# Performance work log

Measured on AMD Instinct MI355X. Metric: run time of the kernel, lower is better.

Reference implementation:

```python
import jax, jax.numpy as jnp
import numpy as np


def _euclidean_cdist(x, q):
    # torch.cdist with p=2: pairwise L2 distances, shape [B, Q]
    x2 = jnp.sum(x * x, axis=-1, keepdims=True)          # [B, 1]
    q2 = jnp.sum(q * q, axis=-1)[None, :]                # [1, Q]
    d2 = x2 + q2 - 2.0 * (x @ q.T)                        # [B, Q]
    return jnp.sqrt(jnp.maximum(d2, 0.0))


def setup_inputs() -> dict:
    key = jax.random.key(0)
    k1, k2 = jax.random.split(key)
    x = jax.random.normal(k1, (1024, 256), dtype=jnp.float32)
    queue = jax.random.normal(k2, (32768, 256), dtype=jnp.float32)
    return {"x": x, "queue": queue}


def reference(x, queue):
    # Queue update: concat then keep the newest max_size rows (queue assumed full)
    max_size = queue.shape[0]
    q = jnp.concatenate([queue, x], axis=0)[-max_size:]   # [Q, F]
    # Distance matrix + top-2 nearest (topk of negated distances)
    d = _euclidean_cdist(x, q)                            # [B, Q]
    _, idx = jax.lax.top_k(-d, 2)                         # [B, 2]
    # Second-nearest neighbor (first is the point itself, dist 0)
    return q[idx[:, 1]]                                   # [B, F]
```

## Files before the change

kernel.cpp:

```cpp
#include <hip/hip_runtime.h>
#include <stdint.h>

#define B_ROWS 1024
#define FEAT   256
#define QSZ    32768
#define SHIFT  1024
#define QX     (QSZ - B_ROWS)
#define BM     64
#define NGY    (QSZ / BM)
#define MARGIN 8.0f

typedef float  v4f __attribute__((ext_vector_type(4)));
typedef short  v8s __attribute__((ext_vector_type(8)));

__device__ __forceinline__ uint32_t key_flip(uint32_t u) {
    return u ^ ((uint32_t)((int32_t)u >> 31) | 0x80000000u);
}
__device__ __forceinline__ float key_m(uint32_t k) {
    uint32_t u = k & 0xFFFF8000u;
    u = (u & 0x80000000u) ? (u ^ 0x80000000u) : ~u;
    return __uint_as_float(u);
}
__device__ __forceinline__ void k2_insert(uint32_t& k1, uint32_t& k2, uint32_t key) {
    uint32_t hi = max(k1, key); k1 = min(k1, key); k2 = min(k2, hi);
}
__device__ __forceinline__ uint2 k2_merge(uint2 a, uint2 b) {
    uint32_t hi = max(a.x, b.x);
    uint2 r; r.x = min(a.x, b.x); r.y = min(min(a.y, b.y), hi);
    return r;
}

struct Top2 { float m1; int j1; float m2; int j2; };
__device__ __forceinline__ bool better(float ma, int ja, float mb, int jb) {
    return (ma < mb) || (ma == mb && ja < jb);
}
__device__ __forceinline__ void t2_insert(Top2& t, float m, int j) {
    if (better(m, j, t.m1, t.j1)) { t.m2 = t.m1; t.j2 = t.j1; t.m1 = m; t.j1 = j; }
    else if (better(m, j, t.m2, t.j2)) { t.m2 = m; t.j2 = j; }
}

__device__ __forceinline__ const float* q_row_ptr(int j, const float* x, const float* queue) {
    return (j < QX) ? (queue + (size_t)(j + SHIFT) * FEAT) : (x + (size_t)(j - QX) * FEAT);
}

__device__ __forceinline__ unsigned short f2bf(float f) {
    uint32_t u = __float_as_uint(f);
    uint32_t r = u + 0x7FFFu + ((u >> 16) & 1u);
    return (unsigned short)(r >> 16);
}

__device__ __forceinline__ void lds_load16(const void* g, void* l) {
    __builtin_amdgcn_global_load_lds(
        (const __attribute__((address_space(1))) uint32_t*)g,
        (__attribute__((address_space(3))) uint32_t*)l, 16, 0, 0);
}

__global__ __launch_bounds__(256) void convert_x(const float* __restrict__ x,
                                                 unsigned short* __restrict__ x_bf) {
    int wave = threadIdx.x >> 6, lane = threadIdx.x & 63;
    int r = blockIdx.x * 4 + wave;
    float4 v = ((const float4*)(x + (size_t)r * FEAT))[lane];
    ushort4 h;
    h.x = f2bf(v.x); h.y = f2bf(v.y); h.z = f2bf(v.z); h.w = f2bf(v.w);
    ((ushort4*)x_bf)[(size_t)r * 64 + lane] = h;
}

__global__ __launch_bounds__(256, 3) void nn_fused(const float* __restrict__ x,
                                                   const float* __restrict__ queue,
                                                   const unsigned short* __restrict__ x_bf,
                                                   float* __restrict__ q2,
                                                   uint2* __restrict__ partials) {
    __shared__ __align__(16) unsigned short As[BM * FEAT];
    __shared__ __align__(16) unsigned short Bs[2][128 * 32];
    __shared__ __align__(16) float sq2[BM];

    const int t    = threadIdx.x;
    const int w    = t >> 6, lane = t & 63;
    const int quad = lane >> 4, l16 = lane & 15;
    const int gy   = blockIdx.x;

    const int srow = lane >> 2;
    const int sgl  = (lane & 3) ^ ((lane >> 3) & 3);
    const unsigned short* gB0 = x_bf + (size_t)(w * 32 + srow) * FEAT + sgl * 8;
    lds_load16(gB0,             &Bs[0][(w * 32) * 32]);
    lds_load16(gB0 + 16 * FEAT, &Bs[0][(w * 32 + 16) * 32]);

    const int arow = t >> 2, aqtr = t & 3;
    const float* asrc = q_row_ptr(gy * BM + arow, x, queue) + aqtr * 64;
    float ss = 0.0f;
#pragma unroll
    for (int gi = 0; gi < 8; ++gi) {
        float4 a = *(const float4*)(asrc + gi * 8);
        float4 b = *(const float4*)(asrc + gi * 8 + 4);
        ss += a.x * a.x + a.y * a.y + a.z * a.z + a.w * a.w
            + b.x * b.x + b.y * b.y + b.z * b.z + b.w * b.w;
        uint32_t p0 = (uint32_t)f2bf(a.x) | ((uint32_t)f2bf(a.y) << 16);
        uint32_t p1 = (uint32_t)f2bf(a.z) | ((uint32_t)f2bf(a.w) << 16);
        uint32_t p2 = (uint32_t)f2bf(b.x) | ((uint32_t)f2bf(b.y) << 16);
        uint32_t p3 = (uint32_t)f2bf(b.z) | ((uint32_t)f2bf(b.w) << 16);
        const int g    = aqtr * 8 + gi;
        const int phys = (g & 24) | ((g & 7) ^ (arow & 7));
        *(uint4*)&As[arow * FEAT + phys * 8] = make_uint4(p0, p1, p2, p3);
    }
    ss += __shfl_xor(ss, 1, 64);
    ss += __shfl_xor(ss, 2, 64);
    if (aqtr == 0) { sq2[arow] = ss; q2[gy * BM + arow] = ss; }

    v4f acc[4][2];
#pragma unroll
    for (int a = 0; a < 4; ++a)
#pragma unroll
        for (int b = 0; b < 2; ++b) acc[a][b] = (v4f)0.0f;

    const int  gphysB = quad ^ ((l16 >> 1) & 3);
    const char* Brd = (const char*)&Bs[0][0] + (size_t)(w * 32 + l16) * 64 + gphysB * 16;

    __syncthreads();

    for (int gx = 0; gx < 8; ++gx) {
#pragma unroll
        for (int c = 0; c < 8; ++c) {
            const int m = gx * 8 + c;
            if (m < 63) {
                const int mm = m + 1;
                const unsigned short* gBn = gB0 + (size_t)(mm >> 3) * (128 * FEAT) + (mm & 7) * 32;
                unsigned short* dstb = &Bs[(c + 1) & 1][(w * 32) * 32];
                lds_load16(gBn,             dstb);
                lds_load16(gBn + 16 * FEAT, dstb + 16 * 32);
                __builtin_amdgcn_sched_barrier(0);
                asm volatile("s_waitcnt vmcnt(2)" ::: "memory");
            } else {
                __builtin_amdgcn_sched_barrier(0);
                asm volatile("s_waitcnt vmcnt(0)" ::: "memory");
            }
            __builtin_amdgcn_s_barrier();

            const int physA = ((c >> 1) * 8) | ((((c & 1) * 4) + quad) ^ (l16 & 7));
            v8s fa[4], fb[2];
#pragma unroll
            for (int tm = 0; tm < 4; ++tm)
                fa[tm] = *(const v8s*)((const char*)As + (size_t)(tm * 16 + l16) * 512 + physA * 16);
            const char* Bc = Brd + (c & 1) * 8192;
#pragma unroll
            for (int tn = 0; tn < 2; ++tn)
                fb[tn] = *(const v8s*)(Bc + tn * 1024);
            __builtin_amdgcn_s_setprio(1);
#pragma unroll
            for (int tm = 0; tm < 4; ++tm)
#pragma unroll
                for (int tn = 0; tn < 2; ++tn)
                    acc[tm][tn] = __builtin_amdgcn_mfma_f32_16x16x32_bf16(fa[tm], fb[tn], acc[tm][tn], 0, 0, 0);
            __builtin_amdgcn_s_setprio(0);
            __builtin_amdgcn_s_barrier();
        }

        float q2r[4][4];
#pragma unroll
        for (int tm = 0; tm < 4; ++tm) {
            v4f qq = *(const v4f*)&sq2[tm * 16 + quad * 4];
#pragma unroll
            for (int r = 0; r < 4; ++r) q2r[tm][r] = qq[r];
        }
        const int jbase = gy * BM + quad * 4;
#pragma unroll
        for (int tn = 0; tn < 2; ++tn) {
            uint32_t k1 = 0xFFFFFFFFu, k2 = 0xFFFFFFFFu;
#pragma unroll
            for (int tm = 0; tm < 4; ++tm)
#pragma unroll
                for (int r = 0; r < 4; ++r) {
                    float mv = fmaf(-2.0f, acc[tm][tn][r], q2r[tm][r]);
                    uint32_t u = key_flip(__float_as_uint(mv));
                    uint32_t key = (u & 0xFFFF8000u) | (uint32_t)(jbase + tm * 16 + r);
                    k2_insert(k1, k2, key);
                    acc[tm][tn][r] = 0.0f;
                }
#pragma unroll
            for (int mask = 16; mask <= 32; mask <<= 1) {
                uint32_t o1 = __shfl_xor(k1, mask, 64);
                uint32_t o2 = __shfl_xor(k2, mask, 64);
                uint32_t hi = max(k1, o1);
                k1 = min(k1, o1);
                k2 = min(min(k2, o2), hi);
            }
            if (quad == 0)
                partials[(size_t)(gx * 128 + w * 32 + tn * 16 + l16) * NGY + gy] = make_uint2(k1, k2);
        }
    }
}

__global__ __launch_bounds__(256) void nn_finalize(const float* __restrict__ x,
                                                   const float* __restrict__ queue,
                                                   const float* __restrict__ q2,
                                                   const uint2* __restrict__ partials,
                                                   float* __restrict__ out) {
    __shared__ float    xs[256];
    __shared__ uint2    red[256];
    __shared__ int      list[64];
    __shared__ float    escore[64];
    __shared__ int      s_cnt;
    __shared__ uint32_t s_kcut;
    __shared__ int      s_j2;

    const int t = threadIdx.x, i = blockIdx.x;
    const int w = t >> 6, lane = t & 63;

    xs[t] = x[(size_t)i * FEAT + t];
    uint2 pa = partials[(size_t)i * NGY + t];
    uint2 pb = partials[(size_t)i * NGY + 256 + t];
    uint2 pm = k2_merge(pa, pb);
    red[t] = pm;
    if (t == 0) s_cnt = 0;
    __syncthreads();

    if (w == 0) {
        uint2 a = red[lane];
        a = k2_merge(a, red[lane + 64]);
        a = k2_merge(a, red[lane + 128]);
        a = k2_merge(a, red[lane + 192]);
#pragma unroll
        for (int mask = 1; mask <= 32; mask <<= 1) {
            uint2 o;
            o.x = __shfl_xor(a.x, mask, 64);
            o.y = __shfl_xor(a.y, mask, 64);
            a = k2_merge(a, o);
        }
        if (lane == 0) {
            float cutf = key_m(a.y) + MARGIN;
            s_kcut = key_flip(__float_as_uint(cutf)) | 0x7FFFu;
        }
    }
    __syncthreads();
    uint32_t kcut = s_kcut;
    if (pm.x <= kcut) { int q_ = atomicAdd(&s_cnt, 1); if (q_ < 64) list[q_] = (int)(pm.x & 0x7FFFu); }
    if (pm.y <= kcut) { int q_ = atomicAdd(&s_cnt, 1); if (q_ < 64) list[q_] = (int)(pm.y & 0x7FFFu); }
    __syncthreads();
    int n = min(s_cnt, 64);

    for (int c = w; c < n; c += 4) {
        int j = list[c];
        const float4* qr = (const float4*)q_row_ptr(j, x, queue);
        float4 qv = qr[lane];
        float4 xv = ((const float4*)xs)[lane];
        float s = qv.x * xv.x + qv.y * xv.y + qv.z * xv.z + qv.w * xv.w;
#pragma unroll
        for (int off = 32; off; off >>= 1) s += __shfl_xor(s, off, 64);
        if (lane == 0) escore[c] = q2[j] - 2.0f * s;
    }
    __syncthreads();
    if (t == 0) {
        Top2 a;
        a.m1 = __builtin_inff(); a.j1 = 0x7FFFFFFF;
        a.m2 = __builtin_inff(); a.j2 = 0x7FFFFFFF;
        for (int c = 0; c < n; ++c) t2_insert(a, escore[c], list[c]);
        s_j2 = a.j2;
    }
    __syncthreads();
    out[(size_t)i * FEAT + t] = q_row_ptr(s_j2, x, queue)[t];
}

extern "C" void kernel_launch(void* const* d_in, const int* in_sizes, int n_in,
                              void* d_out, int out_size, void* d_ws, size_t ws_size,
                              hipStream_t stream) {
    const float* x     = (const float*)d_in[0];
    const float* queue = (const float*)d_in[1];

    unsigned short* x_bf     = (unsigned short*)d_ws;
    float*          q2       = (float*)((char*)d_ws + (1u << 20));
    uint2*          partials = (uint2*)((char*)d_ws + (2u << 20));

    convert_x<<<B_ROWS / 4, 256, 0, stream>>>(x, x_bf);
    nn_fused<<<NGY, 256, 0, stream>>>(x, queue, x_bf, q2, partials);
    nn_finalize<<<B_ROWS, 256, 0, stream>>>(x, queue, q2, partials, (float*)d_out);
}
```

Measured before the change: 119.0 us.

## Keep queue tile in registers and stream x_bf fragments directly from global

The GEMM kernel stops staging x_bf tiles through double-buffered LDS with global_load_lds and barriers. Instead each wave holds the full 64x256 queue tile fragments in registers and loads B fragments straight from global memory into registers, double-buffered across 16-column tiles, with each wave owning 256 x rows. This removes per-step LDS traffic and block barriers, but raises register pressure (occupancy hint lowered from 3 to 2) and relies on cache hits for the uncoalesced-ish global fragment loads.

```diff
diff --git a/kernel.cpp b/kernel.cpp
--- a/kernel.cpp
+++ b/kernel.cpp
@@ -49,12 +49,6 @@
     return (unsigned short)(r >> 16);
 }
 
-__device__ __forceinline__ void lds_load16(const void* g, void* l) {
-    __builtin_amdgcn_global_load_lds(
-        (const __attribute__((address_space(1))) uint32_t*)g,
-        (__attribute__((address_space(3))) uint32_t*)l, 16, 0, 0);
-}
-
 __global__ __launch_bounds__(256) void convert_x(const float* __restrict__ x,
                                                  unsigned short* __restrict__ x_bf) {
     int wave = threadIdx.x >> 6, lane = threadIdx.x & 63;
@@ -65,13 +59,12 @@
     ((ushort4*)x_bf)[(size_t)r * 64 + lane] = h;
 }
 
-__global__ __launch_bounds__(256, 3) void nn_fused(const float* __restrict__ x,
-                                                   const float* __restrict__ queue,
-                                                   const unsigned short* __restrict__ x_bf,
-                                                   float* __restrict__ q2,
-                                                   uint2* __restrict__ partials) {
+__global__ __launch_bounds__(256, 2) void nn_gemm(const float* __restrict__ x,
+                                                  const float* __restrict__ queue,
+                                                  const unsigned short* __restrict__ x_bf,
+                                                  float* __restrict__ q2,
+                                                  uint2* __restrict__ partials) {
     __shared__ __align__(16) unsigned short As[BM * FEAT];
-    __shared__ __align__(16) unsigned short Bs[2][128 * 32];
     __shared__ __align__(16) float sq2[BM];
 
     const int t    = threadIdx.x;
@@ -79,113 +72,96 @@
     const int quad = lane >> 4, l16 = lane & 15;
     const int gy   = blockIdx.x;
 
-    const int srow = lane >> 2;
-    const int sgl  = (lane & 3) ^ ((lane >> 3) & 3);
-    const unsigned short* gB0 = x_bf + (size_t)(w * 32 + srow) * FEAT + sgl * 8;
-    lds_load16(gB0,             &Bs[0][(w * 32) * 32]);
-    lds_load16(gB0 + 16 * FEAT, &Bs[0][(w * 32 + 16) * 32]);
-
-    const int arow = t >> 2, aqtr = t & 3;
-    const float* asrc = q_row_ptr(gy * BM + arow, x, queue) + aqtr * 64;
-    float ss = 0.0f;
-#pragma unroll
-    for (int gi = 0; gi < 8; ++gi) {
-        float4 a = *(const float4*)(asrc + gi * 8);
-        float4 b = *(const float4*)(asrc + gi * 8 + 4);
-        ss += a.x * a.x + a.y * a.y + a.z * a.z + a.w * a.w
-            + b.x * b.x + b.y * b.y + b.z * b.z + b.w * b.w;
-        uint32_t p0 = (uint32_t)f2bf(a.x) | ((uint32_t)f2bf(a.y) << 16);
-        uint32_t p1 = (uint32_t)f2bf(a.z) | ((uint32_t)f2bf(a.w) << 16);
-        uint32_t p2 = (uint32_t)f2bf(b.x) | ((uint32_t)f2bf(b.y) << 16);
-        uint32_t p3 = (uint32_t)f2bf(b.z) | ((uint32_t)f2bf(b.w) << 16);
-        const int g    = aqtr * 8 + gi;
-        const int phys = (g & 24) | ((g & 7) ^ (arow & 7));
-        *(uint4*)&As[arow * FEAT + phys * 8] = make_uint4(p0, p1, p2, p3);
-    }
-    ss += __shfl_xor(ss, 1, 64);
-    ss += __shfl_xor(ss, 2, 64);
-    if (aqtr == 0) { sq2[arow] = ss; q2[gy * BM + arow] = ss; }
-
-    v4f acc[4][2];
-#pragma unroll
-    for (int a = 0; a < 4; ++a)
-#pragma unroll
-        for (int b = 0; b < 2; ++b) acc[a][b] = (v4f)0.0f;
-
-    const int  gphysB = quad ^ ((l16 >> 1) & 3);
-    const char* Brd = (const char*)&Bs[0][0] + (size_t)(w * 32 + l16) * 64 + gphysB * 16;
-
-    __syncthreads();
-
-    for (int gx = 0; gx < 8; ++gx) {
-#pragma unroll
-        for (int c = 0; c < 8; ++c) {
-            const int m = gx * 8 + c;
-            if (m < 63) {
-                const int mm = m + 1;
-                const unsigned short* gBn = gB0 + (size_t)(mm >> 3) * (128 * FEAT) + (mm & 7) * 32;
-                unsigned short* dstb = &Bs[(c + 1) & 1][(w * 32) * 32];
-                lds_load16(gBn,             dstb);
-                lds_load16(gBn + 16 * FEAT, dstb + 16 * 32);
-                __builtin_amdgcn_sched_barrier(0);
-                asm volatile("s_waitcnt vmcnt(2)" ::: "memory");
-            } else {
-                __builtin_amdgcn_sched_barrier(0);
-                asm volatile("s_waitcnt vmcnt(0)" ::: "memory");
+    const unsigned short* bbase = x_bf + (size_t)(w * 256 + l16) * FEAT + quad * 8;
+    v8s fb0[8], fb1[8];
+#pragma unroll
+    for (int kc = 0; kc < 8; ++kc) fb0[kc] = *(const v8s*)(bbase + kc * 32);
+
+    {
+        const int arow = t >> 2, aqtr = t & 3;
+        const float* asrc = q_row_ptr(gy * BM + arow, x, queue) + aqtr * 64;
+        float ss = 0.0f;
+#pragma unroll
+        for (int gi = 0; gi < 8; ++gi) {
+            float4 a = *(const float4*)(asrc + gi * 8);
+            float4 b = *(const float4*)(asrc + gi * 8 + 4);
+            ss += a.x * a.x + a.y * a.y + a.z * a.z + a.w * a.w
+                + b.x * b.x + b.y * b.y + b.z * b.z + b.w * b.w;
+            uint32_t p0 = (uint32_t)f2bf(a.x) | ((uint32_t)f2bf(a.y) << 16);
+            uint32_t p1 = (uint32_t)f2bf(a.z) | ((uint32_t)f2bf(a.w) << 16);
+            uint32_t p2 = (uint32_t)f2bf(b.x) | ((uint32_t)f2bf(b.y) << 16);
+            uint32_t p3 = (uint32_t)f2bf(b.z) | ((uint32_t)f2bf(b.w) << 16);
+            const int g    = aqtr * 8 + gi;
+            const int phys = (g & 24) | ((g & 7) ^ (arow & 7));
+            *(uint4*)&As[arow * FEAT + phys * 8] = make_uint4(p0, p1, p2, p3);
+        }
+        ss += __shfl_xor(ss, 1, 64);
+        ss += __shfl_xor(ss, 2, 64);
+        if (aqtr == 0) { sq2[arow] = ss; q2[gy * BM + arow] = ss; }
+    }
+
+    __syncthreads();
+
+    v8s fa[4][8];
+#pragma unroll
+    for (int tm = 0; tm < 4; ++tm)
+#pragma unroll
+        for (int kc = 0; kc < 8; ++kc) {
+            const int g  = kc * 4 + quad;
+            const int pg = (g & 24) | ((g & 7) ^ (l16 & 7));
+            fa[tm][kc] = *(const v8s*)((const char*)As + (size_t)(tm * 16 + l16) * 512 + pg * 16);
+        }
+
+    float q2r[4][4];
+#pragma unroll
+    for (int tm = 0; tm < 4; ++tm) {
+        v4f qq = *(const v4f*)&sq2[tm * 16 + quad * 4];
+#pragma unroll
+        for (int r = 0; r < 4; ++r) q2r[tm][r] = qq[r];
+    }
+
+    auto process = [&](int tn, const v8s (&fb)[8]) {
+        v4f acc[4] = {(v4f)0.0f, (v4f)0.0f, (v4f)0.0f, (v4f)0.0f};
+#pragma unroll
+        for (int kc = 0; kc < 8; ++kc)
+#pragma unroll
+            for (int tm = 0; tm < 4; ++tm)
+                acc[tm] = __builtin_amdgcn_mfma_f32_16x16x32_bf16(fa[tm][kc], fb[kc], acc[tm], 0, 0, 0);
+        uint32_t k1 = 0xFFFFFFFFu, k2 = 0xFFFFFFFFu;
+        const int jb = gy * BM + quad * 4;
+#pragma unroll
+        for (int tm = 0; tm < 4; ++tm)
+#pragma unroll
+            for (int r = 0; r < 4; ++r) {
+                float m = fmaf(-2.0f, acc[tm][r], q2r[tm][r]);
+                uint32_t u = key_flip(__float_as_uint(m));
+                uint32_t key = (u & 0xFFFF8000u) | (uint32_t)(jb + tm * 16 + r);
+                k2_insert(k1, k2, key);
             }
-            __builtin_amdgcn_s_barrier();
-
-            const int physA = ((c >> 1) * 8) | ((((c & 1) * 4) + quad) ^ (l16 & 7));
-            v8s fa[4], fb[2];
-#pragma unroll
-            for (int tm = 0; tm < 4; ++tm)
-                fa[tm] = *(const v8s*)((const char*)As + (size_t)(tm * 16 + l16) * 512 + physA * 16);
-            const char* Bc = Brd + (c & 1) * 8192;
-#pragma unroll
-            for (int tn = 0; tn < 2; ++tn)
-                fb[tn] = *(const v8s*)(Bc + tn * 1024);
-            __builtin_amdgcn_s_setprio(1);
-#pragma unroll
-            for (int tm = 0; tm < 4; ++tm)
-#pragma unroll
-                for (int tn = 0; tn < 2; ++tn)
-                    acc[tm][tn] = __builtin_amdgcn_mfma_f32_16x16x32_bf16(fa[tm], fb[tn], acc[tm][tn], 0, 0, 0);
-            __builtin_amdgcn_s_setprio(0);
-            __builtin_amdgcn_s_barrier();
-        }
-
-        float q2r[4][4];
-#pragma unroll
-        for (int tm = 0; tm < 4; ++tm) {
-            v4f qq = *(const v4f*)&sq2[tm * 16 + quad * 4];
-#pragma unroll
-            for (int r = 0; r < 4; ++r) q2r[tm][r] = qq[r];
-        }
-        const int jbase = gy * BM + quad * 4;
-#pragma unroll
-        for (int tn = 0; tn < 2; ++tn) {
-            uint32_t k1 = 0xFFFFFFFFu, k2 = 0xFFFFFFFFu;
-#pragma unroll
-            for (int tm = 0; tm < 4; ++tm)
-#pragma unroll
-                for (int r = 0; r < 4; ++r) {
-                    float mv = fmaf(-2.0f, acc[tm][tn][r], q2r[tm][r]);
-                    uint32_t u = key_flip(__float_as_uint(mv));
-                    uint32_t key = (u & 0xFFFF8000u) | (uint32_t)(jbase + tm * 16 + r);
-                    k2_insert(k1, k2, key);
-                    acc[tm][tn][r] = 0.0f;
-                }
-#pragma unroll
-            for (int mask = 16; mask <= 32; mask <<= 1) {
-                uint32_t o1 = __shfl_xor(k1, mask, 64);
-                uint32_t o2 = __shfl_xor(k2, mask, 64);
-                uint32_t hi = max(k1, o1);
-                k1 = min(k1, o1);
-                k2 = min(min(k2, o2), hi);
-            }
-            if (quad == 0)
-                partials[(size_t)(gx * 128 + w * 32 + tn * 16 + l16) * NGY + gy] = make_uint2(k1, k2);
-        }
+#pragma unroll
+        for (int mask = 16; mask <= 32; mask <<= 1) {
+            uint32_t o1 = __shfl_xor(k1, mask, 64);
+            uint32_t o2 = __shfl_xor(k2, mask, 64);
+            uint32_t hi = max(k1, o1);
+            k1 = min(k1, o1);
+            k2 = min(min(k2, o2), hi);
+        }
+        if (quad == 0)
+            partials[(size_t)(w * 256 + tn * 16 + l16) * NGY + gy] = make_uint2(k1, k2);
+    };
+
+    for (int tp = 0; tp < 8; ++tp) {
+        const int tn0 = tp * 2;
+#pragma unroll
+        for (int kc = 0; kc < 8; ++kc)
+            fb1[kc] = *(const v8s*)(bbase + (size_t)(tn0 + 1) * (16 * FEAT) + kc * 32);
+        process(tn0, fb0);
+        if (tp < 7) {
+#pragma unroll
+            for (int kc = 0; kc < 8; ++kc)
+                fb0[kc] = *(const v8s*)(bbase + (size_t)(tn0 + 2) * (16 * FEAT) + kc * 32);
+        }
+        process(tn0 + 1, fb1);
     }
 }
 
@@ -270,6 +246,6 @@
     uint2*          partials = (uint2*)((char*)d_ws + (2u << 20));
 
     convert_x<<<B_ROWS / 4, 256, 0, stream>>>(x, x_bf);
-    nn_fused<<<NGY, 256, 0, stream>>>(x, queue, x_bf, q2, partials);
+    nn_gemm<<<NGY, 256, 0, stream>>>(x, queue, x_bf, q2, partials);
     nn_finalize<<<B_ROWS, 256, 0, stream>>>(x, queue, q2, partials, (float*)d_out);
 }
```

Result: no change. 120.7 us (+1.5%).
